# Optimization experiments

Measured on AMD Instinct MI355X. Metric: run time of the kernel, lower is better.

## Reference

```python
import jax, jax.numpy as jnp
import numpy as np

NUM_GROUPS = 25000  # ppr_idx[-1] + 1, fixed for jit-static segment_sum
E = 400000
NUM_FEATURES = 256
HIDDEN = 256
NUM_CLASSES = 64
HEAD_SIZE = 32


def setup_inputs() -> dict:
    key = jax.random.key(0)
    ks = jax.random.split(key, 10)
    source_attr = jax.random.normal(ks[0], (E, NUM_FEATURES), dtype=jnp.float32)
    neighbor_attr = jax.random.normal(ks[1], (E, NUM_FEATURES), dtype=jnp.float32)
    ppr_scores = jax.random.uniform(ks[2], (E,), dtype=jnp.float32)
    ppr_idx = jnp.sort(jax.random.randint(ks[3], (E,), 0, NUM_GROUPS))
    ppr_idx = ppr_idx.at[-1].set(NUM_GROUPS - 1)  # dim_size = ppr_idx[-1] + 1
    neighbor_idx = jax.random.randint(ks[4], (E,), 0, NUM_GROUPS)
    # MLP weights (Linear bias=False); stored as [in, out]
    def w(k, fan_in, fan_out):
        lim = 1.0 / np.sqrt(fan_in)
        return jax.random.uniform(k, (fan_in, fan_out), minval=-lim, maxval=lim, dtype=jnp.float32)
    W0 = w(ks[5], NUM_FEATURES, HIDDEN)
    W1 = w(ks[6], HIDDEN, HIDDEN)
    W2 = w(ks[7], HIDDEN, NUM_CLASSES)
    Wqk = w(ks[8], NUM_CLASSES, HEAD_SIZE)
    Wk = w(ks[9], NUM_CLASSES, HEAD_SIZE)
    return {"source_attr": source_attr, "neighbor_attr": neighbor_attr,
            "ppr_scores": ppr_scores, "ppr_idx": ppr_idx, "neighbor_idx": neighbor_idx,
            "W0": W0, "W1": W1, "W2": W2, "Wqk": Wqk, "Wk": Wk}


def _mlp(X, W0, W1, W2):
    # dropout = 0 -> identity; Linear bias=False
    h = X @ W0
    h = jax.nn.relu(h) @ W1
    h = jax.nn.relu(h) @ W2
    return h  # [E, num_classes]


def reference(source_attr, neighbor_attr, ppr_scores, ppr_idx, neighbor_idx,
              W0, W1, W2, Wqk, Wk):
    x_source = _mlp(source_attr, W0, W1, W2)     # [E, C]
    x_neighbor = _mlp(neighbor_attr, W0, W1, W2)  # [E, C]
    q = x_source @ Wqk                            # [E, H]
    k = x_neighbor @ Wk                           # [E, H]
    e_attn = jax.nn.sigmoid(jnp.sum(q * k, axis=-1))  # [E]
    weighted = x_neighbor * (e_attn * ppr_scores)[:, None]  # [E, C]
    out = jax.ops.segment_sum(weighted, ppr_idx, num_segments=NUM_GROUPS)  # [G, C]
    return out
```

## Files before the change

kernel.cpp:

```cpp
#include <hip/hip_runtime.h>

typedef __attribute__((ext_vector_type(8))) short short8;
typedef __attribute__((ext_vector_type(4))) float floatx4;
typedef __attribute__((ext_vector_type(4))) unsigned short us4;

#define LDA 264
#define LDX 72

__device__ inline unsigned short f2bf(float f) {
  unsigned u = __float_as_uint(f);
  u = (u + 0x7fffu + ((u >> 16) & 1u)) >> 16;
  return (unsigned short)u;
}
__device__ inline float bf2f(unsigned short h) {
  return __uint_as_float(((unsigned)h) << 16);
}

__global__ void prep_weights(const float* __restrict__ W0, const float* __restrict__ W1,
                             const float* __restrict__ W2, const float* __restrict__ Wqk,
                             const float* __restrict__ Wk,
                             unsigned short* __restrict__ Wt0, unsigned short* __restrict__ Wt1,
                             unsigned short* __restrict__ Wt2, unsigned short* __restrict__ Wqkt,
                             unsigned short* __restrict__ Wkt) {
  int t = blockIdx.x * blockDim.x + threadIdx.x;
  if (t < 65536) {
    int n = t >> 8, k = t & 255;
    Wt0[t] = f2bf(W0[k * 256 + n]);
    Wt1[t] = f2bf(W1[k * 256 + n]);
  }
  if (t < 16384) {
    int n = t >> 8, k = t & 255;
    Wt2[t] = f2bf(W2[k * 64 + n]);
  }
  if (t < 2048) {
    int n = t >> 6, k = t & 63;
    Wqkt[t] = f2bf(Wqk[k * 32 + n]);
    Wkt[t]  = f2bf(Wk[k * 32 + n]);
  }
}

__device__ inline void layer256(const unsigned short* src, unsigned short* dst,
                                const unsigned short* __restrict__ Wt,
                                int wave, int col, int quad) {
  floatx4 acc[4][4];
#pragma unroll
  for (int i = 0; i < 4; ++i)
#pragma unroll
    for (int j = 0; j < 4; ++j) acc[i][j] = (floatx4)0.0f;
  const int nbase = wave * 64;
#pragma unroll
  for (int ks = 0; ks < 8; ++ks) {
    const int k0 = ks * 32 + quad * 8;
    short8 bf[4], af[4];
#pragma unroll
    for (int nt = 0; nt < 4; ++nt)
      bf[nt] = *(const short8*)(Wt + (nbase + nt * 16 + col) * 256 + k0);
#pragma unroll
    for (int mt = 0; mt < 4; ++mt)
      af[mt] = *(const short8*)(src + (mt * 16 + col) * LDA + k0);
#pragma unroll
    for (int mt = 0; mt < 4; ++mt)
#pragma unroll
      for (int nt = 0; nt < 4; ++nt)
        acc[mt][nt] = __builtin_amdgcn_mfma_f32_16x16x32_bf16(af[mt], bf[nt], acc[mt][nt], 0, 0, 0);
  }
#pragma unroll
  for (int mt = 0; mt < 4; ++mt)
#pragma unroll
    for (int nt = 0; nt < 4; ++nt) {
      const int c = nbase + nt * 16 + col;
#pragma unroll
      for (int r = 0; r < 4; ++r) {
        float v = acc[mt][nt][r];
        v = v > 0.0f ? v : 0.0f;
        dst[(mt * 16 + quad * 4 + r) * LDA + c] = f2bf(v);
      }
    }
}

__device__ inline void layer64(const unsigned short* src, unsigned short* xdst,
                               const unsigned short* __restrict__ Wt2,
                               int wave, int col, int quad) {
  floatx4 acc[4];
#pragma unroll
  for (int nt = 0; nt < 4; ++nt) acc[nt] = (floatx4)0.0f;
#pragma unroll
  for (int ks = 0; ks < 8; ++ks) {
    const int k0 = ks * 32 + quad * 8;
    short8 a = *(const short8*)(src + (wave * 16 + col) * LDA + k0);
#pragma unroll
    for (int nt = 0; nt < 4; ++nt) {
      short8 b = *(const short8*)(Wt2 + (nt * 16 + col) * 256 + k0);
      acc[nt] = __builtin_amdgcn_mfma_f32_16x16x32_bf16(a, b, acc[nt], 0, 0, 0);
    }
  }
#pragma unroll
  for (int nt = 0; nt < 4; ++nt)
#pragma unroll
    for (int r = 0; r < 4; ++r)
      xdst[(wave * 16 + quad * 4 + r) * LDX + nt * 16 + col] = f2bf(acc[nt][r]);
}

__device__ inline void qkgemm(const unsigned short* x, const unsigned short* __restrict__ Wqt,
                              floatx4 acc[2], int wave, int col, int quad) {
  acc[0] = (floatx4)0.0f;
  acc[1] = (floatx4)0.0f;
#pragma unroll
  for (int ks = 0; ks < 2; ++ks) {
    const int k0 = ks * 32 + quad * 8;
    short8 a = *(const short8*)(x + (wave * 16 + col) * LDX + k0);
#pragma unroll
    for (int nt = 0; nt < 2; ++nt) {
      short8 b = *(const short8*)(Wqt + (nt * 16 + col) * 64 + k0);
      acc[nt] = __builtin_amdgcn_mfma_f32_16x16x32_bf16(a, b, acc[nt], 0, 0, 0);
    }
  }
}

template <bool IS_SRC>
__global__ __launch_bounds__(256, 2) void mlp_fused(
    const float* __restrict__ attr, const float* __restrict__ ppr_scores,
    const int* __restrict__ ppr_idx,
    const unsigned short* __restrict__ Wt0, const unsigned short* __restrict__ Wt1,
    const unsigned short* __restrict__ Wt2, const unsigned short* __restrict__ Wqt,
    float* __restrict__ qbuf, float* __restrict__ out) {
  __shared__ alignas(16) unsigned short bufA[64 * LDA];
  __shared__ alignas(16) unsigned short bufB[64 * LDA];
  __shared__ float escale[64];
  __shared__ int gid[64];

  const int t = threadIdx.x;
  const int lane = t & 63;
  const int wave = t >> 6;
  const int col = lane & 15;
  const int quad = lane >> 4;
  const long rowbase = (long)blockIdx.x * 64;

#pragma unroll
  for (int it = 0; it < 16; ++it) {
    int flat = it * 1024 + t * 4;
    int row = flat >> 8, c = flat & 255;
    const float4 v = *(const float4*)(attr + (rowbase + row) * 256 + c);
    us4 p;
    p.x = f2bf(v.x); p.y = f2bf(v.y); p.z = f2bf(v.z); p.w = f2bf(v.w);
    *(us4*)(bufA + row * LDA + c) = p;
  }
  if (!IS_SRC && t < 64) gid[t] = ppr_idx[rowbase + t];
  __syncthreads();

  layer256(bufA, bufB, Wt0, wave, col, quad);
  __syncthreads();
  layer256(bufB, bufA, Wt1, wave, col, quad);
  __syncthreads();
  layer64(bufA, bufB, Wt2, wave, col, quad);
  __syncthreads();

  floatx4 acc[2];
  qkgemm(bufB, Wqt, acc, wave, col, quad);

  if (IS_SRC) {
#pragma unroll
    for (int nt = 0; nt < 2; ++nt)
#pragma unroll
      for (int r = 0; r < 4; ++r) {
        long erow = rowbase + wave * 16 + quad * 4 + r;
        qbuf[erow * 32 + nt * 16 + col] = acc[nt][r];
      }
  } else {
    float part[4] = {0.f, 0.f, 0.f, 0.f};
#pragma unroll
    for (int nt = 0; nt < 2; ++nt)
#pragma unroll
      for (int r = 0; r < 4; ++r) {
        long erow = rowbase + wave * 16 + quad * 4 + r;
        part[r] += qbuf[erow * 32 + nt * 16 + col] * acc[nt][r];
      }
#pragma unroll
    for (int r = 0; r < 4; ++r) {
      float s = part[r];
      s += __shfl_xor(s, 1);
      s += __shfl_xor(s, 2);
      s += __shfl_xor(s, 4);
      s += __shfl_xor(s, 8);
      if (col == 0) {
        int lrow = wave * 16 + quad * 4 + r;
        float sig = 1.0f / (1.0f + __expf(-s));
        escale[lrow] = sig * ppr_scores[rowbase + lrow];
      }
    }
    __syncthreads();
    const int c = t & 63;
    const int r0 = (t >> 6) * 16;
    float run = 0.0f;
    int cur = gid[r0];
#pragma unroll
    for (int i = 0; i < 16; ++i) {
      int row = r0 + i;
      int g = gid[row];
      float v = bf2f(bufB[row * LDX + c]) * escale[row];
      if (g != cur) {
        atomicAdd(out + (long)cur * 64 + c, run);
        run = 0.0f;
        cur = g;
      }
      run += v;
    }
    atomicAdd(out + (long)cur * 64 + c, run);
  }
}

extern "C" void kernel_launch(void* const* d_in, const int* in_sizes, int n_in,
                              void* d_out, int out_size, void* d_ws, size_t ws_size,
                              hipStream_t stream) {
  const float* src_attr = (const float*)d_in[0];
  const float* nbr_attr = (const float*)d_in[1];
  const float* ppr      = (const float*)d_in[2];
  const int*   pidx     = (const int*)d_in[3];
  const float* W0  = (const float*)d_in[5];
  const float* W1  = (const float*)d_in[6];
  const float* W2  = (const float*)d_in[7];
  const float* Wqk = (const float*)d_in[8];
  const float* Wk  = (const float*)d_in[9];
  float* out = (float*)d_out;
  const int E = in_sizes[2];

  char* ws = (char*)d_ws;
  float* qbuf = (float*)ws;
  size_t off = (size_t)E * 32 * sizeof(float);
  unsigned short* Wt0  = (unsigned short*)(ws + off); off += 65536 * 2;
  unsigned short* Wt1  = (unsigned short*)(ws + off); off += 65536 * 2;
  unsigned short* Wt2  = (unsigned short*)(ws + off); off += 16384 * 2;
  unsigned short* Wqkt = (unsigned short*)(ws + off); off += 2048 * 2;
  unsigned short* Wkt  = (unsigned short*)(ws + off); off += 2048 * 2;

  hipMemsetAsync(d_out, 0, (size_t)out_size * sizeof(float), stream);
  prep_weights<<<256, 256, 0, stream>>>(W0, W1, W2, Wqk, Wk, Wt0, Wt1, Wt2, Wqkt, Wkt);

  const int blocks = E / 64;
  mlp_fused<true><<<blocks, 256, 0, stream>>>(src_attr, ppr, pidx, Wt0, Wt1, Wt2, Wqkt, qbuf, out);
  mlp_fused<false><<<blocks, 256, 0, stream>>>(nbr_attr, ppr, pidx, Wt0, Wt1, Wt2, Wkt, qbuf, out);
}
```

Measured before the change: 1.327 ms.

## Fuse source and neighbor MLPs into one kernel and software-pipeline fragment loads

Merges the two per-side MLP launches into a single kernel. Each block runs the source MLP, keeps q in registers, then runs the neighbor MLP on the same rows, which removes the E×32 float qbuf write and read through global memory. The GEMM inner loops now prefetch weight and activation fragments one and two k-steps ahead into rotating register buffers to overlap loads with MFMA work. Register pressure rises from the extra fragment buffers and from the live q accumulators, which could hurt occupancy under the 256x2 launch bound.

```diff
diff --git a/kernel.cpp b/kernel.cpp
--- a/kernel.cpp
+++ b/kernel.cpp
@@ -39,7 +39,7 @@
   }
 }
 
-__device__ inline void layer256(const unsigned short* src, unsigned short* dst,
+__device__ inline void layer256(const unsigned short* __restrict__ src, unsigned short* __restrict__ dst,
                                 const unsigned short* __restrict__ Wt,
                                 int wave, int col, int quad) {
   floatx4 acc[4][4];
@@ -48,22 +48,36 @@
 #pragma unroll
     for (int j = 0; j < 4; ++j) acc[i][j] = (floatx4)0.0f;
   const int nbase = wave * 64;
+  const unsigned short* wb = Wt + (nbase + col) * 256 + quad * 8;
+  const unsigned short* ab = src + col * LDA + quad * 8;
+
+  short8 af[2][4], bf[3][4];
+#pragma unroll
+  for (int nt = 0; nt < 4; ++nt) bf[0][nt] = *(const short8*)(wb + nt * 4096);
+#pragma unroll
+  for (int nt = 0; nt < 4; ++nt) bf[1][nt] = *(const short8*)(wb + nt * 4096 + 32);
+#pragma unroll
+  for (int mt = 0; mt < 4; ++mt) af[0][mt] = *(const short8*)(ab + mt * 16 * LDA);
+
 #pragma unroll
   for (int ks = 0; ks < 8; ++ks) {
-    const int k0 = ks * 32 + quad * 8;
-    short8 bf[4], af[4];
-#pragma unroll
-    for (int nt = 0; nt < 4; ++nt)
-      bf[nt] = *(const short8*)(Wt + (nbase + nt * 16 + col) * 256 + k0);
+    if (ks + 2 < 8) {
+#pragma unroll
+      for (int nt = 0; nt < 4; ++nt)
+        bf[(ks + 2) % 3][nt] = *(const short8*)(wb + nt * 4096 + (ks + 2) * 32);
+    }
+    if (ks + 1 < 8) {
+#pragma unroll
+      for (int mt = 0; mt < 4; ++mt)
+        af[(ks + 1) & 1][mt] = *(const short8*)(ab + mt * 16 * LDA + (ks + 1) * 32);
+    }
 #pragma unroll
     for (int mt = 0; mt < 4; ++mt)
-      af[mt] = *(const short8*)(src + (mt * 16 + col) * LDA + k0);
-#pragma unroll
-    for (int mt = 0; mt < 4; ++mt)
 #pragma unroll
       for (int nt = 0; nt < 4; ++nt)
-        acc[mt][nt] = __builtin_amdgcn_mfma_f32_16x16x32_bf16(af[mt], bf[nt], acc[mt][nt], 0, 0, 0);
-  }
+        acc[mt][nt] = __builtin_amdgcn_mfma_f32_16x16x32_bf16(af[ks & 1][mt], bf[ks % 3][nt], acc[mt][nt], 0, 0, 0);
+  }
+
 #pragma unroll
   for (int mt = 0; mt < 4; ++mt)
 #pragma unroll
@@ -78,21 +92,34 @@
     }
 }
 
-__device__ inline void layer64(const unsigned short* src, unsigned short* xdst,
+__device__ inline void layer64(const unsigned short* __restrict__ src, unsigned short* __restrict__ xdst,
                                const unsigned short* __restrict__ Wt2,
                                int wave, int col, int quad) {
   floatx4 acc[4];
 #pragma unroll
   for (int nt = 0; nt < 4; ++nt) acc[nt] = (floatx4)0.0f;
+  const unsigned short* wb = Wt2 + col * 256 + quad * 8;
+  const unsigned short* ab = src + (wave * 16 + col) * LDA + quad * 8;
+
+  short8 af[2];
+  short8 bf[3][4];
+#pragma unroll
+  for (int nt = 0; nt < 4; ++nt) bf[0][nt] = *(const short8*)(wb + nt * 4096);
+#pragma unroll
+  for (int nt = 0; nt < 4; ++nt) bf[1][nt] = *(const short8*)(wb + nt * 4096 + 32);
+  af[0] = *(const short8*)(ab);
+
 #pragma unroll
   for (int ks = 0; ks < 8; ++ks) {
-    const int k0 = ks * 32 + quad * 8;
-    short8 a = *(const short8*)(src + (wave * 16 + col) * LDA + k0);
-#pragma unroll
-    for (int nt = 0; nt < 4; ++nt) {
-      short8 b = *(const short8*)(Wt2 + (nt * 16 + col) * 256 + k0);
-      acc[nt] = __builtin_amdgcn_mfma_f32_16x16x32_bf16(a, b, acc[nt], 0, 0, 0);
-    }
+    if (ks + 2 < 8) {
+#pragma unroll
+      for (int nt = 0; nt < 4; ++nt)
+        bf[(ks + 2) % 3][nt] = *(const short8*)(wb + nt * 4096 + (ks + 2) * 32);
+    }
+    if (ks + 1 < 8) af[(ks + 1) & 1] = *(const short8*)(ab + (ks + 1) * 32);
+#pragma unroll
+    for (int nt = 0; nt < 4; ++nt)
+      acc[nt] = __builtin_amdgcn_mfma_f32_16x16x32_bf16(af[ks & 1], bf[ks % 3][nt], acc[nt], 0, 0, 0);
   }
 #pragma unroll
   for (int nt = 0; nt < 4; ++nt)
@@ -101,7 +128,7 @@
       xdst[(wave * 16 + quad * 4 + r) * LDX + nt * 16 + col] = f2bf(acc[nt][r]);
 }
 
-__device__ inline void qkgemm(const unsigned short* x, const unsigned short* __restrict__ Wqt,
+__device__ inline void qkgemm(const unsigned short* __restrict__ x, const unsigned short* __restrict__ Wqt,
                               floatx4 acc[2], int wave, int col, int quad) {
   acc[0] = (floatx4)0.0f;
   acc[1] = (floatx4)0.0f;
@@ -117,13 +144,25 @@
   }
 }
 
-template <bool IS_SRC>
-__global__ __launch_bounds__(256, 2) void mlp_fused(
-    const float* __restrict__ attr, const float* __restrict__ ppr_scores,
-    const int* __restrict__ ppr_idx,
+__device__ inline void stage_tile(const float* __restrict__ attr, unsigned short* __restrict__ buf,
+                                  long rowbase, int t) {
+#pragma unroll
+  for (int it = 0; it < 16; ++it) {
+    int flat = it * 1024 + t * 4;
+    int row = flat >> 8, c = flat & 255;
+    const float4 v = *(const float4*)(attr + (rowbase + row) * 256 + c);
+    us4 p;
+    p.x = f2bf(v.x); p.y = f2bf(v.y); p.z = f2bf(v.z); p.w = f2bf(v.w);
+    *(us4*)(buf + row * LDA + c) = p;
+  }
+}
+
+__global__ __launch_bounds__(256, 2) void fused_all(
+    const float* __restrict__ sattr, const float* __restrict__ nattr,
+    const float* __restrict__ ppr_scores, const int* __restrict__ ppr_idx,
     const unsigned short* __restrict__ Wt0, const unsigned short* __restrict__ Wt1,
-    const unsigned short* __restrict__ Wt2, const unsigned short* __restrict__ Wqt,
-    float* __restrict__ qbuf, float* __restrict__ out) {
+    const unsigned short* __restrict__ Wt2, const unsigned short* __restrict__ Wqkt,
+    const unsigned short* __restrict__ Wkt, float* __restrict__ out) {
   __shared__ alignas(16) unsigned short bufA[64 * LDA];
   __shared__ alignas(16) unsigned short bufB[64 * LDA];
   __shared__ float escale[64];
@@ -136,77 +175,62 @@
   const int quad = lane >> 4;
   const long rowbase = (long)blockIdx.x * 64;
 
-#pragma unroll
-  for (int it = 0; it < 16; ++it) {
-    int flat = it * 1024 + t * 4;
-    int row = flat >> 8, c = flat & 255;
-    const float4 v = *(const float4*)(attr + (rowbase + row) * 256 + c);
-    us4 p;
-    p.x = f2bf(v.x); p.y = f2bf(v.y); p.z = f2bf(v.z); p.w = f2bf(v.w);
-    *(us4*)(bufA + row * LDA + c) = p;
-  }
-  if (!IS_SRC && t < 64) gid[t] = ppr_idx[rowbase + t];
+  stage_tile(sattr, bufA, rowbase, t);
+  if (t < 64) gid[t] = ppr_idx[rowbase + t];
   __syncthreads();
 
-  layer256(bufA, bufB, Wt0, wave, col, quad);
+  layer256(bufA, bufB, Wt0, wave, col, quad);   __syncthreads();
+  layer256(bufB, bufA, Wt1, wave, col, quad);   __syncthreads();
+  layer64(bufA, bufB, Wt2, wave, col, quad);    __syncthreads();
+
+  floatx4 qa[2];
+  qkgemm(bufB, Wqkt, qa, wave, col, quad);
+
+  stage_tile(nattr, bufA, rowbase, t);
   __syncthreads();
-  layer256(bufB, bufA, Wt1, wave, col, quad);
+
+  layer256(bufA, bufB, Wt0, wave, col, quad);   __syncthreads();
+  layer256(bufB, bufA, Wt1, wave, col, quad);   __syncthreads();
+  layer64(bufA, bufB, Wt2, wave, col, quad);    __syncthreads();
+
+  floatx4 ka[2];
+  qkgemm(bufB, Wkt, ka, wave, col, quad);
+
+  float part[4];
+#pragma unroll
+  for (int r = 0; r < 4; ++r) part[r] = qa[0][r] * ka[0][r] + qa[1][r] * ka[1][r];
+#pragma unroll
+  for (int r = 0; r < 4; ++r) {
+    float s = part[r];
+    s += __shfl_xor(s, 1);
+    s += __shfl_xor(s, 2);
+    s += __shfl_xor(s, 4);
+    s += __shfl_xor(s, 8);
+    if (col == 0) {
+      int lrow = wave * 16 + quad * 4 + r;
+      float sig = 1.0f / (1.0f + __expf(-s));
+      escale[lrow] = sig * ppr_scores[rowbase + lrow];
+    }
+  }
   __syncthreads();
-  layer64(bufA, bufB, Wt2, wave, col, quad);
-  __syncthreads();
-
-  floatx4 acc[2];
-  qkgemm(bufB, Wqt, acc, wave, col, quad);
-
-  if (IS_SRC) {
-#pragma unroll
-    for (int nt = 0; nt < 2; ++nt)
-#pragma unroll
-      for (int r = 0; r < 4; ++r) {
-        long erow = rowbase + wave * 16 + quad * 4 + r;
-        qbuf[erow * 32 + nt * 16 + col] = acc[nt][r];
-      }
-  } else {
-    float part[4] = {0.f, 0.f, 0.f, 0.f};
-#pragma unroll
-    for (int nt = 0; nt < 2; ++nt)
-#pragma unroll
-      for (int r = 0; r < 4; ++r) {
-        long erow = rowbase + wave * 16 + quad * 4 + r;
-        part[r] += qbuf[erow * 32 + nt * 16 + col] * acc[nt][r];
-      }
-#pragma unroll
-    for (int r = 0; r < 4; ++r) {
-      float s = part[r];
-      s += __shfl_xor(s, 1);
-      s += __shfl_xor(s, 2);
-      s += __shfl_xor(s, 4);
-      s += __shfl_xor(s, 8);
-      if (col == 0) {
-        int lrow = wave * 16 + quad * 4 + r;
-        float sig = 1.0f / (1.0f + __expf(-s));
-        escale[lrow] = sig * ppr_scores[rowbase + lrow];
-      }
-    }
-    __syncthreads();
-    const int c = t & 63;
-    const int r0 = (t >> 6) * 16;
-    float run = 0.0f;
-    int cur = gid[r0];
-#pragma unroll
-    for (int i = 0; i < 16; ++i) {
-      int row = r0 + i;
-      int g = gid[row];
-      float v = bf2f(bufB[row * LDX + c]) * escale[row];
-      if (g != cur) {
-        atomicAdd(out + (long)cur * 64 + c, run);
-        run = 0.0f;
-        cur = g;
-      }
-      run += v;
-    }
-    atomicAdd(out + (long)cur * 64 + c, run);
-  }
+
+  const int c = t & 63;
+  const int r0 = (t >> 6) * 16;
+  float run = 0.0f;
+  int cur = gid[r0];
+#pragma unroll
+  for (int i = 0; i < 16; ++i) {
+    int row = r0 + i;
+    int g = gid[row];
+    float v = bf2f(bufB[row * LDX + c]) * escale[row];
+    if (g != cur) {
+      atomicAdd(out + (long)cur * 64 + c, run);
+      run = 0.0f;
+      cur = g;
+    }
+    run += v;
+  }
+  atomicAdd(out + (long)cur * 64 + c, run);
 }
 
 extern "C" void kernel_launch(void* const* d_in, const int* in_sizes, int n_in,
@@ -225,8 +249,7 @@
   const int E = in_sizes[2];
 
   char* ws = (char*)d_ws;
-  float* qbuf = (float*)ws;
-  size_t off = (size_t)E * 32 * sizeof(float);
+  size_t off = 0;
   unsigned short* Wt0  = (unsigned short*)(ws + off); off += 65536 * 2;
   unsigned short* Wt1  = (unsigned short*)(ws + off); off += 65536 * 2;
   unsigned short* Wt2  = (unsigned short*)(ws + off); off += 16384 * 2;
@@ -237,6 +260,6 @@
   prep_weights<<<256, 256, 0, stream>>>(W0, W1, W2, Wqk, Wk, Wt0, Wt1, Wt2, Wqkt, Wkt);
 
   const int blocks = E / 64;
-  mlp_fused<true><<<blocks, 256, 0, stream>>>(src_attr, ppr, pidx, Wt0, Wt1, Wt2, Wqkt, qbuf, out);
-  mlp_fused<false><<<blocks, 256, 0, stream>>>(nbr_attr, ppr, pidx, Wt0, Wt1, Wt2, Wkt, qbuf, out);
-}
+  fused_all<<<blocks, 256, 0, stream>>>(src_attr, nbr_attr, ppr, pidx,
+                                        Wt0, Wt1, Wt2, Wqkt, Wkt, out);
+}
```

After: 1.335 ms. About the same (+0.6%).
